# Optimization experiments

Hardware: AMD Instinct MI355X
Metric: run time of the kernel (lower is better)

Reference implementation:

```python
import jax, jax.numpy as jnp
import numpy as np

NUM_HEADS = 16
HIDDEN = 1024
HEAD_DIM = HIDDEN // NUM_HEADS


def setup_inputs() -> dict:
    key = jax.random.key(0)
    ks = jax.random.split(key, 9)
    B, S, D = 2, 2048, HIDDEN
    s = 1.0 / np.sqrt(D)
    return {
        "x": jax.random.normal(ks[0], (B, S, D), dtype=jnp.float32),
        "Wq": jax.random.normal(ks[1], (D, D), dtype=jnp.float32) * s,
        "bq": jnp.zeros((D,), dtype=jnp.float32),
        "Wk": jax.random.normal(ks[2], (D, D), dtype=jnp.float32) * s,
        "bk": jnp.zeros((D,), dtype=jnp.float32),
        "Wv": jax.random.normal(ks[3], (D, D), dtype=jnp.float32) * s,
        "bv": jnp.zeros((D,), dtype=jnp.float32),
        "Wo": jax.random.normal(ks[4], (D, D), dtype=jnp.float32) * s,
        "bo": jnp.zeros((D,), dtype=jnp.float32),
    }


def reference(x, Wq, bq, Wk, bk, Wv, bv, Wo, bo):
    B, S, D = x.shape
    H, Hd = NUM_HEADS, HEAD_DIM
    # projections -> [B, H, S, Hd]
    def proj(W, b):
        return (x @ W + b).reshape(B, S, H, Hd).transpose(0, 2, 1, 3)
    q = proj(Wq, bq)
    k = proj(Wk, bk)
    v = proj(Wv, bv)
    scores = jnp.einsum('bhqd,bhkd->bhqk', q, k) / jnp.sqrt(jnp.float32(Hd))
    p_attn = jax.nn.softmax(scores, axis=-1)  # dropout = identity (eval)
    ctx = jnp.einsum('bhqk,bhkd->bhqd', p_attn, v)
    attn_mean = jnp.mean(p_attn, axis=1)  # [B, S, S]
    out = ctx.transpose(0, 2, 1, 3).reshape(B, S, D) @ Wo + bo
    return out, attn_mean
```

## Files before the change

kernel.cpp:

```cpp
#include <hip/hip_runtime.h>
#include <math.h>

#define NUM_HEADS 16
#define HEAD_DIM  64
#define HIDDEN    1024
#define BATCH     2
#define SEQ       2048

#define QSCALE 0.1803368801111204f

typedef short bf16x8 __attribute__((ext_vector_type(8)));
typedef short short4v __attribute__((ext_vector_type(4)));
typedef float f32x4 __attribute__((ext_vector_type(4)));

#if __has_builtin(__builtin_amdgcn_exp2f)
#define EXP2F __builtin_amdgcn_exp2f
#else
#define EXP2F exp2f
#endif

__device__ __forceinline__ short f2bf(float f) {
    union { float f; unsigned int u; } x; x.f = f;
    unsigned int r = x.u + 0x7fffu + ((x.u >> 16) & 1u);
    return (short)(r >> 16);
}

__device__ __forceinline__ unsigned int pack_bf16_trunc(float lo, float hi) {
    return __builtin_amdgcn_perm(__float_as_uint(hi), __float_as_uint(lo), 0x07060302u);
}

__device__ __forceinline__ void async16(const void* g, void* l) {
    __builtin_amdgcn_global_load_lds(
        (const __attribute__((address_space(1))) void*)g,
        (__attribute__((address_space(3))) void*)l, 16, 0, 0);
}

__global__ __launch_bounds__(256)
void prep_kernel(const float* __restrict__ x,
                 const float* __restrict__ Wq, const float* __restrict__ Wk,
                 const float* __restrict__ Wv, const float* __restrict__ Wo,
                 short* __restrict__ xb, short* __restrict__ Wt4)
{
    __shared__ float t[64][65];
    const int tid = threadIdx.x;
    const int bid = blockIdx.x;
    if (bid < 4096) {
        size_t i = ((size_t)bid * 256 + tid) * 4;
        float4 v = *(const float4*)&x[i];
        short4v o;
        o.x = f2bf(v.x); o.y = f2bf(v.y); o.z = f2bf(v.z); o.w = f2bf(v.w);
        *(short4v*)&xb[i] = o;
        return;
    }
    const int tb = bid - 4096;
    const int z  = tb >> 8;
    const int cx = tb & 15, cy = (tb >> 4) & 15;
    const float* W = (z == 0) ? Wq : (z == 1) ? Wk : (z == 2) ? Wv : Wo;
    short* dst = Wt4 + (size_t)z * HIDDEN * HIDDEN;
    const int c0 = cx * 64;
    const int r0 = cy * 64;
    const int cl = tid & 63, rw = tid >> 6;
    #pragma unroll
    for (int p = 0; p < 16; ++p) {
        int row = p * 4 + rw;
        t[row][cl] = W[(size_t)(r0 + row) * HIDDEN + c0 + cl];
    }
    __syncthreads();
    #pragma unroll
    for (int p = 0; p < 16; ++p) {
        int orow = p * 4 + rw;
        dst[(size_t)(c0 + orow) * HIDDEN + r0 + cl] = f2bf(t[cl][orow]);
    }
}

__global__ __launch_bounds__(256)
void qkv_proj_kernel(const short* __restrict__ xb, const short* __restrict__ Wt4,
                     const float* __restrict__ bq, const float* __restrict__ bk,
                     const float* __restrict__ bv,
                     short* __restrict__ Qb, short* __restrict__ Kb,
                     short* __restrict__ Vt)
{
    __shared__ short ldsA[128 * 32];
    __shared__ short ldsB[128 * 32];
    const int tid = threadIdx.x;
    const int lane = tid & 63, w = tid >> 6;
    const int l = lane & 15, q = lane >> 4;
    const int n0 = blockIdx.x * 128;
    const int m0 = blockIdx.y * 128;
    const int z  = blockIdx.z;
    const short* Wt = Wt4 + (size_t)z * HIDDEN * HIDDEN;
    const int wm = (w >> 1) * 64, wn = (w & 1) * 64;
    const int kc = q ^ ((l >> 1) & 3);

    f32x4 acc[4][4];
    #pragma unroll
    for (int i = 0; i < 4; ++i)
        #pragma unroll
        for (int j = 0; j < 4; ++j)
            acc[i][j] = (f32x4){0.f, 0.f, 0.f, 0.f};

    for (int k0 = 0; k0 < HIDDEN; k0 += 32) {
        #pragma unroll
        for (int half = 0; half < 2; ++half) {
            int c = half * 256 + tid;
            int row = c >> 2;
            int kcg = (c & 3) ^ ((row >> 1) & 3);
            async16(xb + (size_t)(m0 + row) * HIDDEN + k0 + kcg * 8, &ldsA[c * 8]);
            async16(Wt + (size_t)(n0 + row) * HIDDEN + k0 + kcg * 8, &ldsB[c * 8]);
        }
        __syncthreads();
        bf16x8 af[4], bfr[4];
        #pragma unroll
        for (int i = 0; i < 4; ++i)
            af[i] = *(const bf16x8*)&ldsA[((wm + 16 * i + l) * 4 + kc) * 8];
        #pragma unroll
        for (int j = 0; j < 4; ++j)
            bfr[j] = *(const bf16x8*)&ldsB[((wn + 16 * j + l) * 4 + kc) * 8];
        #pragma unroll
        for (int i = 0; i < 4; ++i)
            #pragma unroll
            for (int j = 0; j < 4; ++j)
                acc[i][j] = __builtin_amdgcn_mfma_f32_16x16x32_bf16(
                    af[i], bfr[j], acc[i][j], 0, 0, 0);
        __syncthreads();
    }

    const float* bias = (z == 0) ? bq : (z == 1) ? bk : bv;
    const float sc = (z == 0) ? QSCALE : 1.0f;
    if (z < 2) {
        short* Ob = (z == 0) ? Qb : Kb;
        #pragma unroll
        for (int j = 0; j < 4; ++j) {
            int n = n0 + wn + 16 * j + l;
            float bval = bias[n];
            int h = n >> 6, hd = n & 63;
            #pragma unroll
            for (int i = 0; i < 4; ++i) {
                #pragma unroll
                for (int reg = 0; reg < 4; ++reg) {
                    int m = m0 + wm + 16 * i + 4 * q + reg;
                    int b_ = m >> 11, s = m & 2047;
                    Ob[(((size_t)(b_ * NUM_HEADS + h) * SEQ) + s) * HEAD_DIM + hd] =
                        f2bf((acc[i][j][reg] + bval) * sc);
                }
            }
        }
    } else {
        #pragma unroll
        for (int j = 0; j < 4; ++j) {
            int n = n0 + wn + 16 * j + l;
            float bval = bias[n];
            int h = n >> 6, hd = n & 63;
            #pragma unroll
            for (int i = 0; i < 4; ++i) {
                int mb = m0 + wm + 16 * i + 4 * q;
                int b_ = mb >> 11, s = mb & 2047;
                short4v pk;
                #pragma unroll
                for (int reg = 0; reg < 4; ++reg)
                    pk[reg] = f2bf(acc[i][j][reg] + bval);
                *(short4v*)&Vt[(((size_t)(b_ * NUM_HEADS + h) * HEAD_DIM) + hd) * SEQ + s] = pk;
            }
        }
    }
}

__global__ __launch_bounds__(256)
void out_proj_kernel(const short* __restrict__ Cb, const short* __restrict__ Wot,
                     const float* __restrict__ bo, float* __restrict__ out)
{
    __shared__ short ldsA[64 * 32];
    __shared__ short ldsB[128 * 32];
    const int tid = threadIdx.x;
    const int lane = tid & 63, w = tid >> 6;
    const int l = lane & 15, q = lane >> 4;
    const int n0 = blockIdx.x * 128;
    const int m0 = blockIdx.y * 64;
    const int kc = q ^ ((l >> 1) & 3);

    f32x4 acc[4][2];
    #pragma unroll
    for (int i = 0; i < 4; ++i)
        #pragma unroll
        for (int j = 0; j < 2; ++j)
            acc[i][j] = (f32x4){0.f, 0.f, 0.f, 0.f};

    for (int k0 = 0; k0 < HIDDEN; k0 += 32) {
        const int h = k0 >> 6, hdb = k0 & 63;
        {
            int c = tid;
            int row = c >> 2;
            int kcg = (c & 3) ^ ((row >> 1) & 3);
            int m = m0 + row;
            int b_ = m >> 11, s = m & 2047;
            async16(Cb + (((size_t)(b_ * NUM_HEADS + h) * SEQ) + s) * HEAD_DIM + hdb + kcg * 8,
                    &ldsA[c * 8]);
        }
        #pragma unroll
        for (int half = 0; half < 2; ++half) {
            int c = half * 256 + tid;
            int row = c >> 2;
            int kcg = (c & 3) ^ ((row >> 1) & 3);
            async16(Wot + (size_t)(n0 + row) * HIDDEN + k0 + kcg * 8, &ldsB[c * 8]);
        }
        __syncthreads();
        bf16x8 af[4], bfr[2];
        #pragma unroll
        for (int i = 0; i < 4; ++i)
            af[i] = *(const bf16x8*)&ldsA[((16 * i + l) * 4 + kc) * 8];
        #pragma unroll
        for (int j = 0; j < 2; ++j)
            bfr[j] = *(const bf16x8*)&ldsB[((32 * w + 16 * j + l) * 4 + kc) * 8];
        #pragma unroll
        for (int i = 0; i < 4; ++i)
            #pragma unroll
            for (int j = 0; j < 2; ++j)
                acc[i][j] = __builtin_amdgcn_mfma_f32_16x16x32_bf16(
                    af[i], bfr[j], acc[i][j], 0, 0, 0);
        __syncthreads();
    }

    #pragma unroll
    for (int j = 0; j < 2; ++j) {
        int n = n0 + 32 * w + 16 * j + l;
        float bval = bo[n];
        #pragma unroll
        for (int i = 0; i < 4; ++i)
            #pragma unroll
            for (int reg = 0; reg < 4; ++reg) {
                int m = m0 + 16 * i + 4 * q + reg;
                out[(size_t)m * HIDDEN + n] = acc[i][j][reg] + bval;
            }
    }
}

__global__ __launch_bounds__(512, 4)
void flash_kernel(const short* __restrict__ Qb, const short* __restrict__ Kb,
                  const short* __restrict__ Vt, short* __restrict__ Cb,
                  float* __restrict__ Lb)
{
    __shared__ short Ks[64 * 64];
    __shared__ short Vs[64 * 64];
    __shared__ float Xch[4][64][34];

    const int tid = threadIdx.x, lane = tid & 63, w = tid >> 6;
    const int l = lane & 15, q = lane >> 4;
    const int qg = w & 3;
    const int kh = w >> 2;
    const int q0 = blockIdx.x * 128;
    const int Q0 = q0 + qg * 32;
    const int h = blockIdx.y, b = blockIdx.z;
    const size_t base  = (size_t)(b * NUM_HEADS + h) * SEQ * HEAD_DIM;
    const size_t vbase = (size_t)(b * NUM_HEADS + h) * HEAD_DIM * SEQ;

    const int c = tid;
    const int row = c >> 3;
    const int g = ((c & 7) ^ (row & 7)) * 8;
    const short* kp = Kb + base + (size_t)row * HEAD_DIM + g;
    const short* vp = Vt + vbase + (size_t)row * SEQ + g;

    bf16x8 bq[2][2];
    #pragma unroll
    for (int u = 0; u < 2; ++u)
        #pragma unroll
        for (int ks = 0; ks < 2; ++ks)
            bq[u][ks] = *(const bf16x8*)(Qb + base +
                (size_t)(Q0 + 16 * u + l) * HEAD_DIM + 32 * ks + 8 * q);

    const int sw = l & 7;
    int kaddr[2];
    #pragma unroll
    for (int ks = 0; ks < 2; ++ks)
        kaddr[ks] = (32 * kh + l) * 64 + ((4 * ks + q) ^ sw) * 8;
    const int vc0 = 4 * kh + (q >> 1);
    const int vaddr0 = l * 64 + ((vc0      ^ sw) * 8) + 4 * (q & 1);
    const int vaddr1 = l * 64 + (((vc0 + 2) ^ sw) * 8) + 4 * (q & 1);

    f32x4 ctx[2][4];
    #pragma unroll
    for (int u = 0; u < 2; ++u)
        #pragma unroll
        for (int m = 0; m < 4; ++m) ctx[u][m] = (f32x4){0.f, 0.f, 0.f, 0.f};
    float l_part[2] = {0.f, 0.f};

    for (int kt = 0; kt < SEQ; kt += 64) {
        async16(kp, &Ks[c * 8]);
        async16(vp, &Vs[c * 8]);
        kp += 64 * HEAD_DIM;
        vp += 64;
        __syncthreads();

        f32x4 st[2][2];
        #pragma unroll
        for (int u = 0; u < 2; ++u)
            #pragma unroll
            for (int t = 0; t < 2; ++t) st[u][t] = (f32x4){0.f, 0.f, 0.f, 0.f};
        #pragma unroll
        for (int ks = 0; ks < 2; ++ks) {
            #pragma unroll
            for (int t = 0; t < 2; ++t) {
                bf16x8 ak = *(const bf16x8*)&Ks[kaddr[ks] + t * 1024];
                st[0][t] = __builtin_amdgcn_mfma_f32_16x16x32_bf16(ak, bq[0][ks], st[0][t], 0, 0, 0);
                st[1][t] = __builtin_amdgcn_mfma_f32_16x16x32_bf16(ak, bq[1][ks], st[1][t], 0, 0, 0);
            }
        }

        union { unsigned int u32[4]; bf16x8 v; } bp[2];
        #pragma unroll
        for (int u = 0; u < 2; ++u) {
            #pragma unroll
            for (int t = 0; t < 2; ++t) {
                float p0 = EXP2F(st[u][t][0]);
                float p1 = EXP2F(st[u][t][1]);
                float p2 = EXP2F(st[u][t][2]);
                float p3 = EXP2F(st[u][t][3]);
                l_part[u] += (p0 + p1) + (p2 + p3);
                bp[u].u32[2 * t]     = pack_bf16_trunc(p0, p1);
                bp[u].u32[2 * t + 1] = pack_bf16_trunc(p2, p3);
            }
        }

        #pragma unroll
        for (int m = 0; m < 4; ++m) {
            short4v g0 = *(const short4v*)&Vs[vaddr0 + m * 1024];
            short4v g1 = *(const short4v*)&Vs[vaddr1 + m * 1024];
            bf16x8 av = __builtin_shufflevector(g0, g1, 0, 1, 2, 3, 4, 5, 6, 7);
            ctx[0][m] = __builtin_amdgcn_mfma_f32_16x16x32_bf16(av, bp[0].v, ctx[0][m], 0, 0, 0);
            ctx[1][m] = __builtin_amdgcn_mfma_f32_16x16x32_bf16(av, bp[1].v, ctx[1][m], 0, 0, 0);
        }
        __syncthreads();
    }

    if (kh == 1) {
        float* dst = &Xch[qg][lane][0];
        #pragma unroll
        for (int u = 0; u < 2; ++u)
            #pragma unroll
            for (int m = 0; m < 4; ++m)
                #pragma unroll
                for (int r = 0; r < 4; ++r)
                    dst[u * 16 + m * 4 + r] = ctx[u][m][r];
        dst[32] = l_part[0];
        dst[33] = l_part[1];
    }
    __syncthreads();
    if (kh == 0) {
        const float* src = &Xch[qg][lane][0];
        #pragma unroll
        for (int u = 0; u < 2; ++u)
            #pragma unroll
            for (int m = 0; m < 4; ++m)
                #pragma unroll
                for (int r = 0; r < 4; ++r)
                    ctx[u][m][r] += src[u * 16 + m * 4 + r];

        #pragma unroll
        for (int u = 0; u < 2; ++u) {
            float rs = l_part[u] + src[32 + u];
            rs += __shfl_xor(rs, 16);
            rs += __shfl_xor(rs, 32);
            float inv_l = 1.0f / rs;
            int s = Q0 + 16 * u + l;
            #pragma unroll
            for (int t = 0; t < 4; ++t) {
                short4v pk;
                #pragma unroll
                for (int reg = 0; reg < 4; ++reg)
                    pk[reg] = f2bf(ctx[u][t][reg] * inv_l);
                *(short4v*)&Cb[(((size_t)(b * NUM_HEADS + h) * SEQ) + s) * HEAD_DIM + 16 * t + 4 * q] = pk;
            }
            if (q == 0)
                Lb[(size_t)(b * NUM_HEADS + h) * SEQ + s] = rs;
        }
    }
}

__global__ __launch_bounds__(256)
void attn_mean_kernel(const short* __restrict__ Qb, const short* __restrict__ Kb,
                      const float* __restrict__ Lb, float* __restrict__ amean)
{
    __shared__ short Qs[64 * 64];
    __shared__ short Ks[256 * 64];
    __shared__ float Le[64];
    const int tid = threadIdx.x, lane = tid & 63, w = tid >> 6;
    const int l = lane & 15, q = lane >> 4;
    const int k0 = blockIdx.x * 256;
    const int q0 = blockIdx.y * 64;
    const int b  = blockIdx.z;
    const size_t HSTRIDE = (size_t)SEQ * HEAD_DIM;

    const short* qp[2];
    const short* kp[8];
    {
        const size_t base0 = (size_t)(b * NUM_HEADS) * HSTRIDE;
        #pragma unroll
        for (int i = 0; i < 2; ++i) {
            int c = 256 * i + tid;
            int row = c >> 3;
            int g = ((c & 7) ^ (row & 7)) * 8;
            qp[i] = Qb + base0 + (size_t)(q0 + row) * HEAD_DIM + g;
        }
        #pragma unroll
        for (int i = 0; i < 8; ++i) {
            int c = 256 * i + tid;
            int row = c >> 3;
            int g = ((c & 7) ^ (row & 7)) * 8;
            kp[i] = Kb + base0 + (size_t)(k0 + row) * HEAD_DIM + g;
        }
    }

    f32x4 macc[4][4];
    #pragma unroll
    for (int tk = 0; tk < 4; ++tk)
        #pragma unroll
        for (int tq = 0; tq < 4; ++tq)
            macc[tk][tq] = (f32x4){0.f, 0.f, 0.f, 0.f};

    for (int h = 0; h < NUM_HEADS; ++h) {
        #pragma unroll
        for (int i = 0; i < 2; ++i) { async16(qp[i], &Qs[(256 * i + tid) * 8]); qp[i] += HSTRIDE; }
        #pragma unroll
        for (int i = 0; i < 8; ++i) { async16(kp[i], &Ks[(256 * i + tid) * 8]); kp[i] += HSTRIDE; }
        if (tid < 64)
            Le[tid] = 1.0f / Lb[(size_t)(b * NUM_HEADS + h) * SEQ + q0 + tid];
        __syncthreads();

        bf16x8 bq[4][2];
        #pragma unroll
        for (int tq = 0; tq < 4; ++tq)
            #pragma unroll
            for (int ks = 0; ks < 2; ++ks) {
                int cc = (4 * ks + q) ^ (l & 7);
                bq[tq][ks] = *(const bf16x8*)&Qs[((16 * tq + l) * 8 + cc) * 8];
            }

        #pragma unroll
        for (int tk = 0; tk < 4; ++tk) {
            bf16x8 ak[2];
            #pragma unroll
            for (int ks = 0; ks < 2; ++ks) {
                int cc = (4 * ks + q) ^ (l & 7);
                ak[ks] = *(const bf16x8*)&Ks[((64 * w + 16 * tk + l) * 8 + cc) * 8];
            }
            #pragma unroll
            for (int tq = 0; tq < 4; ++tq) {
                f32x4 st = (f32x4){0.f, 0.f, 0.f, 0.f};
                st = __builtin_amdgcn_mfma_f32_16x16x32_bf16(ak[0], bq[tq][0], st, 0, 0, 0);
                st = __builtin_amdgcn_mfma_f32_16x16x32_bf16(ak[1], bq[tq][1], st, 0, 0, 0);
                float li = Le[16 * tq + l];
                #pragma unroll
                for (int reg = 0; reg < 4; ++reg)
                    macc[tk][tq][reg] += EXP2F(st[reg]) * li;
            }
        }
        __syncthreads();
    }

    const float inv_h = 1.0f / (float)NUM_HEADS;
    #pragma unroll
    for (int tq = 0; tq < 4; ++tq) {
        int row_q = q0 + 16 * tq + l;
        #pragma unroll
        for (int tk = 0; tk < 4; ++tk) {
            int col_k = k0 + 64 * w + 16 * tk + 4 * q;
            f32x4 o;
            #pragma unroll
            for (int reg = 0; reg < 4; ++reg) o[reg] = macc[tk][tq][reg] * inv_h;
            *(f32x4*)&amean[((size_t)b * SEQ + row_q) * SEQ + col_k] = o;
        }
    }
}

extern "C" void kernel_launch(void* const* d_in, const int* in_sizes, int n_in,
                              void* d_out, int out_size, void* d_ws, size_t ws_size,
                              hipStream_t stream)
{
    const float* x  = (const float*)d_in[0];
    const float* Wq = (const float*)d_in[1];
    const float* bq = (const float*)d_in[2];
    const float* Wk = (const float*)d_in[3];
    const float* bk = (const float*)d_in[4];
    const float* Wv = (const float*)d_in[5];
    const float* bv = (const float*)d_in[6];
    const float* Wo = (const float*)d_in[7];
    const float* bo = (const float*)d_in[8];

    float* out   = (float*)d_out;
    float* amean = out + (size_t)BATCH * SEQ * HIDDEN;

    const size_t NELEM = (size_t)BATCH * NUM_HEADS * SEQ * HEAD_DIM;
    short* ws  = (short*)d_ws;
    short* xb  = ws;
    short* Wt4 = xb + NELEM;
    short* Qb  = Wt4 + 4 * (size_t)HIDDEN * HIDDEN;
    short* Kb  = Qb + NELEM;
    short* Vt  = Kb + NELEM;
    short* Cb  = Vt + NELEM;
    float* Lb  = (float*)(Cb + NELEM);

    dim3 blk(256);
    prep_kernel<<<dim3(4096 + 1024), blk, 0, stream>>>(x, Wq, Wk, Wv, Wo, xb, Wt4);
    qkv_proj_kernel<<<dim3(8, 32, 3), blk, 0, stream>>>(xb, Wt4, bq, bk, bv, Qb, Kb, Vt);
    flash_kernel<<<dim3(SEQ / 128, NUM_HEADS, BATCH), dim3(512), 0, stream>>>(Qb, Kb, Vt, Cb, Lb);
    attn_mean_kernel<<<dim3(SEQ / 256, SEQ / 64, BATCH), blk, 0, stream>>>(Qb, Kb, Lb, amean);
    out_proj_kernel<<<dim3(8, 64), blk, 0, stream>>>(Cb, Wt4 + 3 * (size_t)HIDDEN * HIDDEN, bo, out);
}
```

Before: 251.4 us.

## Double-buffer LDS tiles with async prefetch across all GEMM and attention kernels

Converts the qkv projection, output projection, flash attention and attention-mean kernels to double-buffered LDS staging. The next tile is issued asynchronously while the current one is computed, using explicit vmcnt waits and barriers in place of __syncthreads. The attention-mean kernel now uses 128-column key tiles instead of 256 to fit two buffers, and reads the inverse row sums directly from global memory. Flash now stores the inverse normaliser rather than the sum, which removes a division per head. Doubling LDS may lower occupancy, and the hand-counted vmcnt values must match the number of loads issued per stage.

New measurement: 253.9 us. Within noise of the previous version (+1.0%).

```diff
diff --git a/kernel.cpp b/kernel.cpp
--- a/kernel.cpp
+++ b/kernel.cpp
@@ -18,6 +18,12 @@
 #else
 #define EXP2F exp2f
 #endif
+
+#define ACQB(N) do { asm volatile("s_waitcnt vmcnt(" #N ")" ::: "memory"); \
+                     __builtin_amdgcn_s_barrier(); } while (0)
+#define RELB()  do { asm volatile("s_waitcnt lgkmcnt(0)" ::: "memory");   \
+                     __builtin_amdgcn_sched_barrier(0);                    \
+                     __builtin_amdgcn_s_barrier(); } while (0)
 
 __device__ __forceinline__ short f2bf(float f) {
     union { float f; unsigned int u; } x; x.f = f;
@@ -80,8 +86,8 @@
                      short* __restrict__ Qb, short* __restrict__ Kb,
                      short* __restrict__ Vt)
 {
-    __shared__ short ldsA[128 * 32];
-    __shared__ short ldsB[128 * 32];
+    __shared__ short ldsA[2][128 * 32];
+    __shared__ short ldsB[2][128 * 32];
     const int tid = threadIdx.x;
     const int lane = tid & 63, w = tid >> 6;
     const int l = lane & 15, q = lane >> 4;
@@ -99,31 +105,40 @@
         for (int j = 0; j < 4; ++j)
             acc[i][j] = (f32x4){0.f, 0.f, 0.f, 0.f};
 
-    for (int k0 = 0; k0 < HIDDEN; k0 += 32) {
+    auto STG = [&](int buf, int t) {
         #pragma unroll
         for (int half = 0; half < 2; ++half) {
             int c = half * 256 + tid;
             int row = c >> 2;
             int kcg = (c & 3) ^ ((row >> 1) & 3);
-            async16(xb + (size_t)(m0 + row) * HIDDEN + k0 + kcg * 8, &ldsA[c * 8]);
-            async16(Wt + (size_t)(n0 + row) * HIDDEN + k0 + kcg * 8, &ldsB[c * 8]);
-        }
-        __syncthreads();
+            async16(xb + (size_t)(m0 + row) * HIDDEN + t * 32 + kcg * 8, &ldsA[buf][c * 8]);
+            async16(Wt + (size_t)(n0 + row) * HIDDEN + t * 32 + kcg * 8, &ldsB[buf][c * 8]);
+        }
+    };
+    auto CMP = [&](int buf) {
         bf16x8 af[4], bfr[4];
         #pragma unroll
         for (int i = 0; i < 4; ++i)
-            af[i] = *(const bf16x8*)&ldsA[((wm + 16 * i + l) * 4 + kc) * 8];
+            af[i] = *(const bf16x8*)&ldsA[buf][((wm + 16 * i + l) * 4 + kc) * 8];
         #pragma unroll
         for (int j = 0; j < 4; ++j)
-            bfr[j] = *(const bf16x8*)&ldsB[((wn + 16 * j + l) * 4 + kc) * 8];
+            bfr[j] = *(const bf16x8*)&ldsB[buf][((wn + 16 * j + l) * 4 + kc) * 8];
         #pragma unroll
         for (int i = 0; i < 4; ++i)
             #pragma unroll
             for (int j = 0; j < 4; ++j)
                 acc[i][j] = __builtin_amdgcn_mfma_f32_16x16x32_bf16(
                     af[i], bfr[j], acc[i][j], 0, 0, 0);
-        __syncthreads();
-    }
+    };
+
+    STG(0, 0); STG(1, 1);
+    ACQB(4);
+    for (int tp = 0; tp < 15; ++tp) {
+        CMP(0); RELB(); STG(0, 2 * tp + 2); ACQB(4);
+        CMP(1); RELB(); STG(1, 2 * tp + 3); ACQB(4);
+    }
+    CMP(0); RELB(); ACQB(0);
+    CMP(1);
 
     const float* bias = (z == 0) ? bq : (z == 1) ? bk : bv;
     const float sc = (z == 0) ? QSCALE : 1.0f;
@@ -169,8 +184,8 @@
 void out_proj_kernel(const short* __restrict__ Cb, const short* __restrict__ Wot,
                      const float* __restrict__ bo, float* __restrict__ out)
 {
-    __shared__ short ldsA[64 * 32];
-    __shared__ short ldsB[128 * 32];
+    __shared__ short ldsA[2][64 * 32];
+    __shared__ short ldsB[2][128 * 32];
     const int tid = threadIdx.x;
     const int lane = tid & 63, w = tid >> 6;
     const int l = lane & 15, q = lane >> 4;
@@ -185,40 +200,49 @@
         for (int j = 0; j < 2; ++j)
             acc[i][j] = (f32x4){0.f, 0.f, 0.f, 0.f};
 
-    for (int k0 = 0; k0 < HIDDEN; k0 += 32) {
-        const int h = k0 >> 6, hdb = k0 & 63;
+    auto STG = [&](int buf, int t) {
         {
             int c = tid;
             int row = c >> 2;
             int kcg = (c & 3) ^ ((row >> 1) & 3);
             int m = m0 + row;
             int b_ = m >> 11, s = m & 2047;
+            int h = t >> 1, hdb = (t & 1) << 5;
             async16(Cb + (((size_t)(b_ * NUM_HEADS + h) * SEQ) + s) * HEAD_DIM + hdb + kcg * 8,
-                    &ldsA[c * 8]);
+                    &ldsA[buf][c * 8]);
         }
         #pragma unroll
         for (int half = 0; half < 2; ++half) {
             int c = half * 256 + tid;
             int row = c >> 2;
             int kcg = (c & 3) ^ ((row >> 1) & 3);
-            async16(Wot + (size_t)(n0 + row) * HIDDEN + k0 + kcg * 8, &ldsB[c * 8]);
-        }
-        __syncthreads();
+            async16(Wot + (size_t)(n0 + row) * HIDDEN + t * 32 + kcg * 8, &ldsB[buf][c * 8]);
+        }
+    };
+    auto CMP = [&](int buf) {
         bf16x8 af[4], bfr[2];
         #pragma unroll
         for (int i = 0; i < 4; ++i)
-            af[i] = *(const bf16x8*)&ldsA[((16 * i + l) * 4 + kc) * 8];
+            af[i] = *(const bf16x8*)&ldsA[buf][((16 * i + l) * 4 + kc) * 8];
         #pragma unroll
         for (int j = 0; j < 2; ++j)
-            bfr[j] = *(const bf16x8*)&ldsB[((32 * w + 16 * j + l) * 4 + kc) * 8];
+            bfr[j] = *(const bf16x8*)&ldsB[buf][((32 * w + 16 * j + l) * 4 + kc) * 8];
         #pragma unroll
         for (int i = 0; i < 4; ++i)
             #pragma unroll
             for (int j = 0; j < 2; ++j)
                 acc[i][j] = __builtin_amdgcn_mfma_f32_16x16x32_bf16(
                     af[i], bfr[j], acc[i][j], 0, 0, 0);
-        __syncthreads();
-    }
+    };
+
+    STG(0, 0); STG(1, 1);
+    ACQB(3);
+    for (int tp = 0; tp < 15; ++tp) {
+        CMP(0); RELB(); STG(0, 2 * tp + 2); ACQB(3);
+        CMP(1); RELB(); STG(1, 2 * tp + 3); ACQB(3);
+    }
+    CMP(0); RELB(); ACQB(0);
+    CMP(1);
 
     #pragma unroll
     for (int j = 0; j < 2; ++j) {
@@ -239,9 +263,9 @@
                   const short* __restrict__ Vt, short* __restrict__ Cb,
                   float* __restrict__ Lb)
 {
-    __shared__ short Ks[64 * 64];
-    __shared__ short Vs[64 * 64];
-    __shared__ float Xch[4][64][34];
+    __shared__ short Ks[2][64 * 64];
+    __shared__ short Vs[2][64 * 64];
+    __shared__ float Xch[4][64][35];
 
     const int tid = threadIdx.x, lane = tid & 63, w = tid >> 6;
     const int l = lane & 15, q = lane >> 4;
@@ -253,20 +277,20 @@
     const size_t base  = (size_t)(b * NUM_HEADS + h) * SEQ * HEAD_DIM;
     const size_t vbase = (size_t)(b * NUM_HEADS + h) * HEAD_DIM * SEQ;
 
+    bf16x8 bq[2][2];
+    #pragma unroll
+    for (int u = 0; u < 2; ++u)
+        #pragma unroll
+        for (int ks = 0; ks < 2; ++ks)
+            bq[u][ks] = *(const bf16x8*)(Qb + base +
+                (size_t)(Q0 + 16 * u + l) * HEAD_DIM + 32 * ks + 8 * q);
+
     const int c = tid;
     const int row = c >> 3;
     const int g = ((c & 7) ^ (row & 7)) * 8;
     const short* kp = Kb + base + (size_t)row * HEAD_DIM + g;
     const short* vp = Vt + vbase + (size_t)row * SEQ + g;
 
-    bf16x8 bq[2][2];
-    #pragma unroll
-    for (int u = 0; u < 2; ++u)
-        #pragma unroll
-        for (int ks = 0; ks < 2; ++ks)
-            bq[u][ks] = *(const bf16x8*)(Qb + base +
-                (size_t)(Q0 + 16 * u + l) * HEAD_DIM + 32 * ks + 8 * q);
-
     const int sw = l & 7;
     int kaddr[2];
     #pragma unroll
@@ -283,13 +307,13 @@
         for (int m = 0; m < 4; ++m) ctx[u][m] = (f32x4){0.f, 0.f, 0.f, 0.f};
     float l_part[2] = {0.f, 0.f};
 
-    for (int kt = 0; kt < SEQ; kt += 64) {
-        async16(kp, &Ks[c * 8]);
-        async16(vp, &Vs[c * 8]);
+    auto STG = [&](int buf) {
+        async16(kp, &Ks[buf][c * 8]);
+        async16(vp, &Vs[buf][c * 8]);
         kp += 64 * HEAD_DIM;
         vp += 64;
-        __syncthreads();
-
+    };
+    auto CMP = [&](int buf) {
         f32x4 st[2][2];
         #pragma unroll
         for (int u = 0; u < 2; ++u)
@@ -299,12 +323,11 @@
         for (int ks = 0; ks < 2; ++ks) {
             #pragma unroll
             for (int t = 0; t < 2; ++t) {
-                bf16x8 ak = *(const bf16x8*)&Ks[kaddr[ks] + t * 1024];
+                bf16x8 ak = *(const bf16x8*)&Ks[buf][kaddr[ks] + t * 1024];
                 st[0][t] = __builtin_amdgcn_mfma_f32_16x16x32_bf16(ak, bq[0][ks], st[0][t], 0, 0, 0);
                 st[1][t] = __builtin_amdgcn_mfma_f32_16x16x32_bf16(ak, bq[1][ks], st[1][t], 0, 0, 0);
             }
         }
-
         union { unsigned int u32[4]; bf16x8 v; } bp[2];
         #pragma unroll
         for (int u = 0; u < 2; ++u) {
@@ -319,17 +342,24 @@
                 bp[u].u32[2 * t + 1] = pack_bf16_trunc(p2, p3);
             }
         }
-
         #pragma unroll
         for (int m = 0; m < 4; ++m) {
-            short4v g0 = *(const short4v*)&Vs[vaddr0 + m * 1024];
-            short4v g1 = *(const short4v*)&Vs[vaddr1 + m * 1024];
+            short4v g0 = *(const short4v*)&Vs[buf][vaddr0 + m * 1024];
+            short4v g1 = *(const short4v*)&Vs[buf][vaddr1 + m * 1024];
             bf16x8 av = __builtin_shufflevector(g0, g1, 0, 1, 2, 3, 4, 5, 6, 7);
             ctx[0][m] = __builtin_amdgcn_mfma_f32_16x16x32_bf16(av, bp[0].v, ctx[0][m], 0, 0, 0);
             ctx[1][m] = __builtin_amdgcn_mfma_f32_16x16x32_bf16(av, bp[1].v, ctx[1][m], 0, 0, 0);
         }
-        __syncthreads();
-    }
+    };
+
+    STG(0); STG(1);
+    ACQB(2);
+    for (int tp = 0; tp < 15; ++tp) {
+        CMP(0); RELB(); STG(0); ACQB(2);
+        CMP(1); RELB(); STG(1); ACQB(2);
+    }
+    CMP(0); RELB(); ACQB(0);
+    CMP(1);
 
     if (kh == 1) {
         float* dst = &Xch[qg][lane][0];
@@ -370,7 +400,7 @@
                 *(short4v*)&Cb[(((size_t)(b * NUM_HEADS + h) * SEQ) + s) * HEAD_DIM + 16 * t + 4 * q] = pk;
             }
             if (q == 0)
-                Lb[(size_t)(b * NUM_HEADS + h) * SEQ + s] = rs;
+                Lb[(size_t)(b * NUM_HEADS + h) * SEQ + s] = inv_l;
         }
     }
 }
@@ -379,51 +409,55 @@
 void attn_mean_kernel(const short* __restrict__ Qb, const short* __restrict__ Kb,
                       const float* __restrict__ Lb, float* __restrict__ amean)
 {
-    __shared__ short Qs[64 * 64];
-    __shared__ short Ks[256 * 64];
-    __shared__ float Le[64];
+    __shared__ short Qs[2][64 * 64];
+    __shared__ short Ks[2][128 * 64];
     const int tid = threadIdx.x, lane = tid & 63, w = tid >> 6;
     const int l = lane & 15, q = lane >> 4;
-    const int k0 = blockIdx.x * 256;
+    const int k0 = blockIdx.x * 128;
     const int q0 = blockIdx.y * 64;
     const int b  = blockIdx.z;
     const size_t HSTRIDE = (size_t)SEQ * HEAD_DIM;
 
     const short* qp[2];
-    const short* kp[8];
+    const short* kp[4];
     {
         const size_t base0 = (size_t)(b * NUM_HEADS) * HSTRIDE;
         #pragma unroll
         for (int i = 0; i < 2; ++i) {
-            int c = 256 * i + tid;
-            int row = c >> 3;
-            int g = ((c & 7) ^ (row & 7)) * 8;
-            qp[i] = Qb + base0 + (size_t)(q0 + row) * HEAD_DIM + g;
-        }
-        #pragma unroll
-        for (int i = 0; i < 8; ++i) {
-            int c = 256 * i + tid;
-            int row = c >> 3;
-            int g = ((c & 7) ^ (row & 7)) * 8;
-            kp[i] = Kb + base0 + (size_t)(k0 + row) * HEAD_DIM + g;
-        }
-    }
-
-    f32x4 macc[4][4];
-    #pragma unroll
-    for (int tk = 0; tk < 4; ++tk)
+            int cc = 256 * i + tid;
+            int row = cc >> 3;
+            int gg = ((cc & 7) ^ (row & 7)) * 8;
+            qp[i] = Qb + base0 + (size_t)(q0 + row) * HEAD_DIM + gg;
+        }
+        #pragma unroll
+        for (int i = 0; i < 4; ++i) {
+            int cc = 256 * i + tid;
+            int row = cc >> 3;
+            int gg = ((cc & 7) ^ (row & 7)) * 8;
+            kp[i] = Kb + base0 + (size_t)(k0 + row) * HEAD_DIM + gg;
+        }
+    }
+
+    f32x4 macc[2][4];
+    #pragma unroll
+    for (int tk = 0; tk < 2; ++tk)
         #pragma unroll
         for (int tq = 0; tq < 4; ++tq)
             macc[tk][tq] = (f32x4){0.f, 0.f, 0.f, 0.f};
 
-    for (int h = 0; h < NUM_HEADS; ++h) {
-        #pragma unroll
-        for (int i = 0; i < 2; ++i) { async16(qp[i], &Qs[(256 * i + tid) * 8]); qp[i] += HSTRIDE; }
-        #pragma unroll
-        for (int i = 0; i < 8; ++i) { async16(kp[i], &Ks[(256 * i + tid) * 8]); kp[i] += HSTRIDE; }
-        if (tid < 64)
-            Le[tid] = 1.0f / Lb[(size_t)(b * NUM_HEADS + h) * SEQ + q0 + tid];
-        __syncthreads();
+    auto STG = [&](int buf) {
+        #pragma unroll
+        for (int i = 0; i < 2; ++i) { async16(qp[i], &Qs[buf][(256 * i + tid) * 8]); qp[i] += HSTRIDE; }
+        #pragma unroll
+        for (int i = 0; i < 4; ++i) { async16(kp[i], &Ks[buf][(256 * i + tid) * 8]); kp[i] += HSTRIDE; }
+    };
+    int hc = 0;
+    auto CMP = [&](int buf) {
+        int h = hc++;
+        float linv[4];
+        #pragma unroll
+        for (int tq = 0; tq < 4; ++tq)
+            linv[tq] = Lb[(size_t)(b * NUM_HEADS + h) * SEQ + q0 + 16 * tq + l];
 
         bf16x8 bq[4][2];
         #pragma unroll
@@ -431,38 +465,45 @@
             #pragma unroll
             for (int ks = 0; ks < 2; ++ks) {
                 int cc = (4 * ks + q) ^ (l & 7);
-                bq[tq][ks] = *(const bf16x8*)&Qs[((16 * tq + l) * 8 + cc) * 8];
-            }
-
-        #pragma unroll
-        for (int tk = 0; tk < 4; ++tk) {
+                bq[tq][ks] = *(const bf16x8*)&Qs[buf][((16 * tq + l) * 8 + cc) * 8];
+            }
+        #pragma unroll
+        for (int tk = 0; tk < 2; ++tk) {
             bf16x8 ak[2];
             #pragma unroll
             for (int ks = 0; ks < 2; ++ks) {
                 int cc = (4 * ks + q) ^ (l & 7);
-                ak[ks] = *(const bf16x8*)&Ks[((64 * w + 16 * tk + l) * 8 + cc) * 8];
+                ak[ks] = *(const bf16x8*)&Ks[buf][((32 * w + 16 * tk + l) * 8 + cc) * 8];
             }
             #pragma unroll
             for (int tq = 0; tq < 4; ++tq) {
                 f32x4 st = (f32x4){0.f, 0.f, 0.f, 0.f};
                 st = __builtin_amdgcn_mfma_f32_16x16x32_bf16(ak[0], bq[tq][0], st, 0, 0, 0);
                 st = __builtin_amdgcn_mfma_f32_16x16x32_bf16(ak[1], bq[tq][1], st, 0, 0, 0);
-                float li = Le[16 * tq + l];
+                float li = linv[tq];
                 #pragma unroll
                 for (int reg = 0; reg < 4; ++reg)
                     macc[tk][tq][reg] += EXP2F(st[reg]) * li;
             }
         }
-        __syncthreads();
-    }
+    };
+
+    STG(0); STG(1);
+    ACQB(6);
+    for (int tp = 0; tp < 7; ++tp) {
+        CMP(0); RELB(); STG(0); ACQB(6);
+        CMP(1); RELB(); STG(1); ACQB(6);
+    }
+    CMP(0); RELB(); ACQB(0);
+    CMP(1);
 
     const float inv_h = 1.0f / (float)NUM_HEADS;
     #pragma unroll
     for (int tq = 0; tq < 4; ++tq) {
         int row_q = q0 + 16 * tq + l;
         #pragma unroll
-        for (int tk = 0; tk < 4; ++tk) {
-            int col_k = k0 + 64 * w + 16 * tk + 4 * q;
+        for (int tk = 0; tk < 2; ++tk) {
+            int col_k = k0 + 32 * w + 16 * tk + 4 * q;
             f32x4 o;
             #pragma unroll
             for (int reg = 0; reg < 4; ++reg) o[reg] = macc[tk][tq][reg] * inv_h;
@@ -502,6 +543,6 @@
     prep_kernel<<<dim3(4096 + 1024), blk, 0, stream>>>(x, Wq, Wk, Wv, Wo, xb, Wt4);
     qkv_proj_kernel<<<dim3(8, 32, 3), blk, 0, stream>>>(xb, Wt4, bq, bk, bv, Qb, Kb, Vt);
     flash_kernel<<<dim3(SEQ / 128, NUM_HEADS, BATCH), dim3(512), 0, stream>>>(Qb, Kb, Vt, Cb, Lb);
-    attn_mean_kernel<<<dim3(SEQ / 256, SEQ / 64, BATCH), blk, 0, stream>>>(Qb, Kb, Lb, amean);
+    attn_mean_kernel<<<dim3(SEQ / 128, SEQ / 64, BATCH), blk, 0, stream>>>(Qb, Kb, Lb, amean);
     out_proj_kernel<<<dim3(8, 64), blk, 0, stream>>>(Cb, Wt4 + 3 * (size_t)HIDDEN * HIDDEN, bo, out);
 }
```
